# Kernel optimization log

Hardware: AMD Instinct MI355X
Metric: run time of the kernel (lower is better)

## Reference

```python
import jax, jax.numpy as jnp
import numpy as np

DEPTH = 64
N_HEAD = 8
FF = 128
EPS = 1e-5


def layer_norm(x, g, b):
    mu = jnp.mean(x, axis=-1, keepdims=True)
    var = jnp.mean((x - mu) ** 2, axis=-1, keepdims=True)
    return (x - mu) * jax.lax.rsqrt(var + EPS) * g + b


def setup_inputs() -> dict:
    key = jax.random.key(0)
    ks = jax.random.split(key, 16)
    B, S, d, h = 4, 512, DEPTH, N_HEAD
    s = 1.0 / np.sqrt(d)
    return {
        "seq": jax.random.normal(ks[0], (B, S, d), jnp.float32),
        "pos_enc": jax.random.normal(ks[1], (B, S, S, d), jnp.float32),
        "Wq": jax.random.normal(ks[2], (d, d * h), jnp.float32) * s,
        "Wk": jax.random.normal(ks[3], (d, d * h), jnp.float32) * s,
        "Wv": jax.random.normal(ks[4], (d, d * h), jnp.float32) * s,
        "Wo": jax.random.normal(ks[5], (d * h, d), jnp.float32) / np.sqrt(d * h),
        "Wp": jax.random.normal(ks[6], (d, h), jnp.float32) * s,
        "bp": jnp.zeros((h,), jnp.float32),
        "W1": jax.random.normal(ks[7], (d, FF), jnp.float32) * s,
        "b1": jnp.zeros((FF,), jnp.float32),
        "W2": jax.random.normal(ks[8], (FF, d), jnp.float32) / np.sqrt(FF),
        "b2": jnp.zeros((d,), jnp.float32),
        "g_att": jnp.ones((d,), jnp.float32),
        "b_att": jnp.zeros((d,), jnp.float32),
        "g_ff": jnp.ones((d,), jnp.float32),
        "b_ff": jnp.zeros((d,), jnp.float32),
    }


def reference(seq, pos_enc, Wq, Wk, Wv, Wo, Wp, bp, W1, b1, W2, b2, g_att, b_att, g_ff, b_ff):
    B, S, d = seq.shape
    h = N_HEAD
    # QKV: [B,S,h,d] -> [B,h,S,d]; head_dim == depth in this module
    q = (seq @ Wq).reshape(B, S, h, d).transpose(0, 2, 1, 3)
    k = (seq @ Wk).reshape(B, S, h, d).transpose(0, 2, 1, 3)
    v = (seq @ Wv).reshape(B, S, h, d).transpose(0, 2, 1, 3)
    a = jnp.einsum('bhid,bhjd->bhij', q, k) / jnp.sqrt(jnp.asarray(d, seq.dtype))
    # additive learned positional bias: [B,S,S,d] @ [d,h] -> [B,S,S,h] -> [B,h,S,S]
    p = jnp.einsum('bijd,dh->bhij', pos_enc, Wp) + bp[None, :, None, None]
    a = jax.nn.softmax(a + p, axis=-1)
    heads = jnp.einsum('bhij,bhjd->bhid', a, v)  # [B,h,S,d]
    o = heads.transpose(0, 2, 1, 3).reshape(B, S, h * d) @ Wo
    x = layer_norm(seq + o, g_att, b_att)
    y = jax.nn.relu(x @ W1 + b1) @ W2 + b2
    return layer_norm(x + y, g_ff, b_ff)
```

## Files before the change

### kernel.cpp

```cpp
#include <hip/hip_runtime.h>
#include <hip/hip_bf16.h>

#define DEPTH 64
#define NH 8
#define SEQL 512
#define BATCH 4
#define FFDIM 128
#define PROJ (DEPTH*NH)
#define LOG2E 1.44269504088896340736f

typedef __hip_bfloat16 bf16;
typedef __attribute__((ext_vector_type(8))) short short8;
typedef __attribute__((ext_vector_type(4))) float floatx4;

__device__ __forceinline__ short f2bs(float f) {
    __hip_bfloat16 h = __float2bfloat16(f);
    return *reinterpret_cast<short*>(&h);
}
__device__ __forceinline__ float bs2f(short s) {
    __hip_bfloat16 h = *reinterpret_cast<__hip_bfloat16*>(&s);
    return __bfloat162float(h);
}

__global__ __launch_bounds__(256) void qkv_kernel(
    const float* __restrict__ seq, const float* __restrict__ Wq,
    const float* __restrict__ Wk, const float* __restrict__ Wv,
    bf16* __restrict__ q, bf16* __restrict__ k, bf16* __restrict__ vT)
{
    __shared__ __align__(16) short sS[64][72];
    __shared__ __align__(16) short sW[128][72];
    __shared__ __align__(16) short sT[128][72];
    int t = threadIdx.x;
    int lane = t & 63, w = t >> 6;
    const float* W; int vflag = 0;
    bf16* out;
    if (blockIdx.z == 0)      { W = Wq; out = q; }
    else if (blockIdx.z == 1) { W = Wk; out = k; }
    else                      { W = Wv; out = vT; vflag = 1; }
    int m0 = blockIdx.x * 64;
    int n0 = blockIdx.y * 128;

    for (int idx = t; idx < 4096; idx += 256) {
        int r = idx >> 6, kk = idx & 63;
        sS[r][kk] = f2bs(seq[(long)(m0 + r)*64 + kk]);
    }
    for (int idx = t; idx < 8192; idx += 256) {
        int kk = idx >> 7, n = idx & 127;
        sW[n][kk] = f2bs(W[kk*512 + n0 + n]);
    }
    __syncthreads();

    int ln = lane & 15, g4 = lane >> 4;
    int mt = w;
    floatx4 acc[2][4];
    #pragma unroll
    for (int nh = 0; nh < 2; nh++)
        #pragma unroll
        for (int nt = 0; nt < 4; nt++) acc[nh][nt] = (floatx4){0.f,0.f,0.f,0.f};
    #pragma unroll
    for (int ks = 0; ks < 2; ks++) {
        short8 af = *(const short8*)&sS[mt*16 + ln][ks*32 + g4*8];
        #pragma unroll
        for (int nh = 0; nh < 2; nh++)
            #pragma unroll
            for (int nt = 0; nt < 4; nt++) {
                short8 bfv = *(const short8*)&sW[nh*64 + nt*16 + ln][ks*32 + g4*8];
                acc[nh][nt] = __builtin_amdgcn_mfma_f32_16x16x32_bf16(af, bfv, acc[nh][nt], 0, 0, 0);
            }
    }

    if (!vflag) {
        #pragma unroll
        for (int nh = 0; nh < 2; nh++)
            #pragma unroll
            for (int nt = 0; nt < 4; nt++)
                #pragma unroll
                for (int r = 0; r < 4; r++) {
                    int grow = m0 + mt*16 + g4*4 + r;
                    int col  = n0 + nh*64 + nt*16 + ln;
                    int b = grow >> 9, s = grow & 511;
                    int h = col >> 6, d = col & 63;
                    out[(((long)(b*8 + h)*512) + s)*64 + d] = __float2bfloat16(acc[nh][nt][r]);
                }
    } else {
        #pragma unroll
        for (int nh = 0; nh < 2; nh++)
            #pragma unroll
            for (int nt = 0; nt < 4; nt++)
                #pragma unroll
                for (int r = 0; r < 4; r++)
                    sT[nh*64 + nt*16 + ln][mt*16 + g4*4 + r] = f2bs(acc[nh][nt][r]);
        __syncthreads();
        int b = m0 >> 9, s0 = m0 & 511;
        for (int idx = t; idx < 1024; idx += 256) {
            int lc = idx >> 3, c8 = idx & 7;
            *(uint4*)(out + ((long)(b*512 + n0 + lc))*512 + s0 + c8*8) =
                *(const uint4*)&sT[lc][c8*8];
        }
    }
}

__global__ __launch_bounds__(256) void pbias_kernel(
    const float* __restrict__ pos, const float* __restrict__ Wp,
    const float* __restrict__ bp, bf16* __restrict__ p)
{
    __shared__ __align__(16) float sW2[4][132];
    __shared__ float sb[8];
    int t = threadIdx.x;
    for (int i = t; i < 512; i += 256) {
        int sub = i >> 7, rest = i & 127;
        int lk = rest >> 3, h = rest & 7;
        int kk = ((lk >> 2) << 4) + sub*4 + (lk & 3);
        sW2[sub][lk*8 + h] = Wp[kk*8 + h];
    }
    if (t < 8) sb[t] = bp[t];
    __syncthreads();

    int sub = t & 3;
    int lrow = t >> 2;
    long row = (long)blockIdx.x*64 + lrow;

    const float4* src = (const float4*)(pos + row*64);
    float4 ch[4];
    #pragma unroll
    for (int i = 0; i < 4; i++) ch[i] = src[i*4 + sub];

    float acc[8];
    #pragma unroll
    for (int h = 0; h < 8; h++) acc[h] = 0.f;
    #pragma unroll
    for (int i = 0; i < 4; i++) {
        #pragma unroll
        for (int e = 0; e < 4; e++) {
            float x = ((const float*)&ch[i])[e];
            int lk = i*4 + e;
            const float4* wr = (const float4*)&sW2[sub][lk*8];
            float4 wa = wr[0], wb = wr[1];
            acc[0] += x*wa.x; acc[1] += x*wa.y; acc[2] += x*wa.z; acc[3] += x*wa.w;
            acc[4] += x*wb.x; acc[5] += x*wb.y; acc[6] += x*wb.z; acc[7] += x*wb.w;
        }
    }
    #pragma unroll
    for (int h = 0; h < 8; h++) {
        acc[h] += __shfl_xor(acc[h], 1, 64);
        acc[h] += __shfl_xor(acc[h], 2, 64);
    }
    int b = (int)(row >> 18);
    int rem = (int)(row & 262143);
    int i = rem >> 9, j = rem & 511;
    int h1 = sub, h2 = sub + 4;
    p[(((long)(b*8 + h1)*512 + i) << 9) + j] = __float2bfloat16(acc[h1] + sb[h1]);
    p[(((long)(b*8 + h2)*512 + i) << 9) + j] = __float2bfloat16(acc[h2] + sb[h2]);
}

__global__ __launch_bounds__(256) void attn_kernel(
    const bf16* __restrict__ q, const bf16* __restrict__ k,
    const bf16* __restrict__ vT, const bf16* __restrict__ p,
    bf16* __restrict__ heads)
{
    __shared__ __align__(16) short sQ[64*72];
    __shared__ __align__(16) short sK[64*72];
    __shared__ __align__(16) short sV[64*72];
    __shared__ __align__(16) short sP[4][16*72];

    int t = threadIdx.x;
    int lane = t & 63, w = t >> 6;
    int bid = blockIdx.x;
    int it = bid & 7;
    int bh = bid >> 3;
    int i0 = it*64;

    const bf16* qb = q + ((long)bh*SEQL + i0)*DEPTH;
    const bf16* kb = k + (long)bh*SEQL*DEPTH;
    const bf16* vb = vT + (long)bh*DEPTH*SEQL;
    const bf16* pb = p + ((long)bh*SEQL + i0)*SEQL;

    for (int c = t; c < 512; c += 256) {
        int r = c >> 3, c8 = c & 7;
        *(uint4*)((char*)sQ + r*144 + c8*16) = *(const uint4*)(qb + r*64 + c8*8);
    }

    int ln = lane & 15, g4 = lane >> 4;
    float lsum[4];
    floatx4 oacc[4];
    #pragma unroll
    for (int r = 0; r < 4; r++) lsum[r] = 0.f;
    #pragma unroll
    for (int ds = 0; ds < 4; ds++) oacc[ds] = (floatx4){0.f,0.f,0.f,0.f};

    for (int jt = 0; jt < 8; jt++) {
        __syncthreads();
        int j0 = jt*64;
        for (int c = t; c < 512; c += 256) {
            int r = c >> 3, c8 = c & 7;
            *(uint4*)((char*)sK + r*144 + c8*16) = *(const uint4*)(kb + (long)(j0 + r)*64 + c8*8);
        }
        for (int c = t; c < 512; c += 256) {
            int r = c >> 3, c8 = c & 7;
            *(uint4*)((char*)sV + r*144 + c8*16) = *(const uint4*)(vb + (long)r*512 + j0 + c8*8);
        }
        __syncthreads();

        floatx4 sacc[4];
        #pragma unroll
        for (int js = 0; js < 4; js++) sacc[js] = (floatx4){0.f,0.f,0.f,0.f};
        #pragma unroll
        for (int kk = 0; kk < 2; kk++) {
            short8 aq = *(const short8*)((const char*)sQ + (w*16 + ln)*144 + kk*64 + g4*16);
            #pragma unroll
            for (int js = 0; js < 4; js++) {
                short8 bk = *(const short8*)((const char*)sK + (js*16 + ln)*144 + kk*64 + g4*16);
                sacc[js] = __builtin_amdgcn_mfma_f32_16x16x32_bf16(aq, bk, sacc[js], 0, 0, 0);
            }
        }
        #pragma unroll
        for (int js = 0; js < 4; js++)
            #pragma unroll
            for (int r = 0; r < 4; r++) {
                int gi = w*16 + g4*4 + r;
                int gj = j0 + js*16 + ln;
                float pv = __bfloat162float(pb[(long)gi*SEQL + gj]);
                float e = exp2f((sacc[js][r]*0.125f + pv)*LOG2E);
                lsum[r] += e;
                sP[w][(g4*4 + r)*72 + js*16 + ln] = f2bs(e);
            }
        #pragma unroll
        for (int kk = 0; kk < 2; kk++) {
            short8 ap = *(const short8*)((const char*)sP[w] + ln*144 + kk*64 + g4*16);
            #pragma unroll
            for (int ds = 0; ds < 4; ds++) {
                short8 bv = *(const short8*)((const char*)sV + (ds*16 + ln)*144 + kk*64 + g4*16);
                oacc[ds] = __builtin_amdgcn_mfma_f32_16x16x32_bf16(ap, bv, oacc[ds], 0, 0, 0);
            }
        }
    }

    #pragma unroll
    for (int r = 0; r < 4; r++)
        #pragma unroll
        for (int m = 1; m < 16; m <<= 1) lsum[r] += __shfl_xor(lsum[r], m, 64);

    int b = bh >> 3, h = bh & 7;
    #pragma unroll
    for (int ds = 0; ds < 4; ds++)
        #pragma unroll
        for (int r = 0; r < 4; r++) {
            float val = oacc[ds][r] / lsum[r];
            int gi = i0 + w*16 + g4*4 + r;
            int col = h*64 + ds*16 + ln;
            heads[((long)b*SEQL + gi)*PROJ + col] = __float2bfloat16(val);
        }
}

__global__ __launch_bounds__(256) void tail_kernel(
    const bf16* __restrict__ heads, const float* __restrict__ Wo,
    const float* __restrict__ seq, const float* __restrict__ g_att,
    const float* __restrict__ b_att, const float* __restrict__ W1,
    const float* __restrict__ b1, const float* __restrict__ W2,
    const float* __restrict__ b2, const float* __restrict__ g_ff,
    const float* __restrict__ b_ff, float* __restrict__ out)
{
    __shared__ __align__(16) short sH[4][520];
    __shared__ float sX[4][68];
    __shared__ float sHid[4][132];
    int t = threadIdx.x;
    int w = t >> 6, lane = t & 63;
    long g0 = (long)blockIdx.x*4;
    {
        int r = t >> 6, c8 = t & 63;
        *(uint4*)((char*)&sH[r][0] + c8*16) = *(const uint4*)(heads + (g0 + r)*PROJ + c8*8);
    }
    float acc = 0.f;
    #pragma unroll 8
    for (int kk = 0; kk < PROJ; kk++) {
        float hv = bs2f(sH[w][kk]);
        acc += hv * Wo[kk*DEPTH + lane];
    }
    long row = g0 + w;
    float x0 = acc + seq[row*DEPTH + lane];
    float s1 = x0, s2 = x0*x0;
    #pragma unroll
    for (int m = 1; m < 64; m <<= 1) { s1 += __shfl_xor(s1, m, 64); s2 += __shfl_xor(s2, m, 64); }
    float mu = s1*(1.f/64.f);
    float var = s2*(1.f/64.f) - mu*mu;
    float rstd = rsqrtf(var + 1e-5f);
    float xn = (x0 - mu)*rstd*g_att[lane] + b_att[lane];
    sX[w][lane] = xn;

    float h0 = b1[lane], h1 = b1[lane + 64];
    #pragma unroll 8
    for (int kk = 0; kk < DEPTH; kk++) {
        float xv = sX[w][kk];
        h0 += xv * W1[kk*FFDIM + lane];
        h1 += xv * W1[kk*FFDIM + 64 + lane];
    }
    h0 = fmaxf(h0, 0.f); h1 = fmaxf(h1, 0.f);
    sHid[w][lane] = h0; sHid[w][lane + 64] = h1;

    float acc2 = b2[lane];
    #pragma unroll 8
    for (int kk = 0; kk < FFDIM; kk++)
        acc2 += sHid[w][kk] * W2[kk*DEPTH + lane];

    float z = xn + acc2;
    float t1 = z, t2 = z*z;
    #pragma unroll
    for (int m = 1; m < 64; m <<= 1) { t1 += __shfl_xor(t1, m, 64); t2 += __shfl_xor(t2, m, 64); }
    float mu2 = t1*(1.f/64.f);
    float var2 = t2*(1.f/64.f) - mu2*mu2;
    float rstd2 = rsqrtf(var2 + 1e-5f);
    out[row*DEPTH + lane] = (z - mu2)*rstd2*g_ff[lane] + b_ff[lane];
}

extern "C" void kernel_launch(void* const* d_in, const int* in_sizes, int n_in,
                              void* d_out, int out_size, void* d_ws, size_t ws_size,
                              hipStream_t stream) {
    const float* seq   = (const float*)d_in[0];
    const float* pos   = (const float*)d_in[1];
    const float* Wq    = (const float*)d_in[2];
    const float* Wk    = (const float*)d_in[3];
    const float* Wv    = (const float*)d_in[4];
    const float* Wo    = (const float*)d_in[5];
    const float* Wp    = (const float*)d_in[6];
    const float* bp    = (const float*)d_in[7];
    const float* W1    = (const float*)d_in[8];
    const float* b1    = (const float*)d_in[9];
    const float* W2    = (const float*)d_in[10];
    const float* b2    = (const float*)d_in[11];
    const float* g_att = (const float*)d_in[12];
    const float* b_att = (const float*)d_in[13];
    const float* g_ff  = (const float*)d_in[14];
    const float* b_ff  = (const float*)d_in[15];
    float* outp = (float*)d_out;

    bf16* qb  = (bf16*)d_ws;
    bf16* kb  = qb + 1048576;
    bf16* vTb = kb + 1048576;
    bf16* pb  = vTb + 1048576;
    bf16* hb  = pb + 8388608;

    qkv_kernel  <<<dim3(32, 4, 3), 256, 0, stream>>>(seq, Wq, Wk, Wv, qb, kb, vTb);
    pbias_kernel<<<16384,          256, 0, stream>>>(pos, Wp, bp, pb);
    attn_kernel <<<256,            256, 0, stream>>>(qb, kb, vTb, pb, hb);
    tail_kernel <<<512,            256, 0, stream>>>(hb, Wo, seq, g_att, b_att,
                                                     W1, b1, W2, b2, g_ff, b_ff, outp);
}
```

Before: 112.9 us.

## Merge QKV and pos-bias kernels, shrink attention tiles, prefetch bias, batch tail rows

Merges the QKV projection and the positional-bias projection into one launch, with block ranges dispatched by block index and shared memory overlapped through a union. This removes one kernel launch and lets both parts run concurrently. The attention kernel switches to 32-row query tiles with 128 threads, giving twice as many blocks, and prefetches the next tile's bias values into registers during the K/V loop. The tail kernel has each wave process two rows so every Wo/W1/W2 weight load is reused twice. Together these add register pressure and change occupancy.

```diff
diff --git a/kernel.cpp b/kernel.cpp
--- a/kernel.cpp
+++ b/kernel.cpp
@@ -22,160 +22,164 @@
     return __bfloat162float(h);
 }
 
-__global__ __launch_bounds__(256) void qkv_kernel(
+__global__ __launch_bounds__(256) void front_kernel(
     const float* __restrict__ seq, const float* __restrict__ Wq,
     const float* __restrict__ Wk, const float* __restrict__ Wv,
-    bf16* __restrict__ q, bf16* __restrict__ k, bf16* __restrict__ vT)
+    const float* __restrict__ pos, const float* __restrict__ Wp,
+    const float* __restrict__ bp,
+    bf16* __restrict__ q, bf16* __restrict__ k, bf16* __restrict__ vT,
+    bf16* __restrict__ p)
 {
-    __shared__ __align__(16) short sS[64][72];
-    __shared__ __align__(16) short sW[128][72];
-    __shared__ __align__(16) short sT[128][72];
+    __shared__ __align__(16) union {
+        struct { short sS[64][72]; short sW[128][72]; } g;
+        struct { float sW2[4][132]; float sb[8]; } pb;
+    } U;
     int t = threadIdx.x;
-    int lane = t & 63, w = t >> 6;
-    const float* W; int vflag = 0;
-    bf16* out;
-    if (blockIdx.z == 0)      { W = Wq; out = q; }
-    else if (blockIdx.z == 1) { W = Wk; out = k; }
-    else                      { W = Wv; out = vT; vflag = 1; }
-    int m0 = blockIdx.x * 64;
-    int n0 = blockIdx.y * 128;
-
-    for (int idx = t; idx < 4096; idx += 256) {
-        int r = idx >> 6, kk = idx & 63;
-        sS[r][kk] = f2bs(seq[(long)(m0 + r)*64 + kk]);
-    }
-    for (int idx = t; idx < 8192; idx += 256) {
-        int kk = idx >> 7, n = idx & 127;
-        sW[n][kk] = f2bs(W[kk*512 + n0 + n]);
-    }
-    __syncthreads();
-
-    int ln = lane & 15, g4 = lane >> 4;
-    int mt = w;
-    floatx4 acc[2][4];
-    #pragma unroll
-    for (int nh = 0; nh < 2; nh++)
-        #pragma unroll
-        for (int nt = 0; nt < 4; nt++) acc[nh][nt] = (floatx4){0.f,0.f,0.f,0.f};
-    #pragma unroll
-    for (int ks = 0; ks < 2; ks++) {
-        short8 af = *(const short8*)&sS[mt*16 + ln][ks*32 + g4*8];
+    int bid = blockIdx.x;
+
+    if (bid < 384) {
+        int lane = t & 63, w = t >> 6;
+        int z = bid >> 7, rem = bid & 127;
+        int mi = rem & 31, ni = rem >> 5;
+        const float* W; int vflag = 0; bf16* out;
+        if (z == 0)      { W = Wq; out = q; }
+        else if (z == 1) { W = Wk; out = k; }
+        else             { W = Wv; out = vT; vflag = 1; }
+        int m0 = mi * 64;
+        int n0 = ni * 128;
+
+        for (int idx = t; idx < 4096; idx += 256) {
+            int r = idx >> 6, kk = idx & 63;
+            U.g.sS[r][kk] = f2bs(seq[(long)(m0 + r)*64 + kk]);
+        }
+        for (int idx = t; idx < 8192; idx += 256) {
+            int kk = idx >> 7, n = idx & 127;
+            U.g.sW[n][kk] = f2bs(W[kk*512 + n0 + n]);
+        }
+        __syncthreads();
+
+        int ln = lane & 15, g4 = lane >> 4;
+        int mt = w;
+        floatx4 acc[2][4];
         #pragma unroll
         for (int nh = 0; nh < 2; nh++)
             #pragma unroll
-            for (int nt = 0; nt < 4; nt++) {
-                short8 bfv = *(const short8*)&sW[nh*64 + nt*16 + ln][ks*32 + g4*8];
-                acc[nh][nt] = __builtin_amdgcn_mfma_f32_16x16x32_bf16(af, bfv, acc[nh][nt], 0, 0, 0);
-            }
-    }
-
-    if (!vflag) {
-        #pragma unroll
-        for (int nh = 0; nh < 2; nh++)
-            #pragma unroll
-            for (int nt = 0; nt < 4; nt++)
+            for (int nt = 0; nt < 4; nt++) acc[nh][nt] = (floatx4){0.f,0.f,0.f,0.f};
+        #pragma unroll
+        for (int ks = 0; ks < 2; ks++) {
+            short8 af = *(const short8*)&U.g.sS[mt*16 + ln][ks*32 + g4*8];
+            #pragma unroll
+            for (int nh = 0; nh < 2; nh++)
                 #pragma unroll
-                for (int r = 0; r < 4; r++) {
-                    int grow = m0 + mt*16 + g4*4 + r;
-                    int col  = n0 + nh*64 + nt*16 + ln;
-                    int b = grow >> 9, s = grow & 511;
-                    int h = col >> 6, d = col & 63;
-                    out[(((long)(b*8 + h)*512) + s)*64 + d] = __float2bfloat16(acc[nh][nt][r]);
+                for (int nt = 0; nt < 4; nt++) {
+                    short8 bfv = *(const short8*)&U.g.sW[nh*64 + nt*16 + ln][ks*32 + g4*8];
+                    acc[nh][nt] = __builtin_amdgcn_mfma_f32_16x16x32_bf16(af, bfv, acc[nh][nt], 0, 0, 0);
                 }
+        }
+
+        if (!vflag) {
+            #pragma unroll
+            for (int nh = 0; nh < 2; nh++)
+                #pragma unroll
+                for (int nt = 0; nt < 4; nt++)
+                    #pragma unroll
+                    for (int r = 0; r < 4; r++) {
+                        int grow = m0 + mt*16 + g4*4 + r;
+                        int col  = n0 + nh*64 + nt*16 + ln;
+                        int b = grow >> 9, s = grow & 511;
+                        int h = col >> 6, d = col & 63;
+                        out[(((long)(b*8 + h)*512) + s)*64 + d] = __float2bfloat16(acc[nh][nt][r]);
+                    }
+        } else {
+            __syncthreads();
+            short (*sT)[72] = U.g.sW;
+            #pragma unroll
+            for (int nh = 0; nh < 2; nh++)
+                #pragma unroll
+                for (int nt = 0; nt < 4; nt++)
+                    #pragma unroll
+                    for (int r = 0; r < 4; r++)
+                        sT[nh*64 + nt*16 + ln][mt*16 + g4*4 + r] = f2bs(acc[nh][nt][r]);
+            __syncthreads();
+            int b = m0 >> 9, s0 = m0 & 511;
+            for (int idx = t; idx < 1024; idx += 256) {
+                int lc = idx >> 3, c8 = idx & 7;
+                *(uint4*)(out + ((long)(b*512 + n0 + lc))*512 + s0 + c8*8) =
+                    *(const uint4*)&sT[lc][c8*8];
+            }
+        }
     } else {
-        #pragma unroll
-        for (int nh = 0; nh < 2; nh++)
-            #pragma unroll
-            for (int nt = 0; nt < 4; nt++)
-                #pragma unroll
-                for (int r = 0; r < 4; r++)
-                    sT[nh*64 + nt*16 + ln][mt*16 + g4*4 + r] = f2bs(acc[nh][nt][r]);
+        int pid = bid - 384;
+        for (int i = t; i < 512; i += 256) {
+            int sub = i >> 7, rest = i & 127;
+            int lk = rest >> 3, h = rest & 7;
+            int kk = ((lk >> 2) << 4) + sub*4 + (lk & 3);
+            U.pb.sW2[sub][lk*8 + h] = Wp[kk*8 + h];
+        }
+        if (t < 8) U.pb.sb[t] = bp[t];
         __syncthreads();
-        int b = m0 >> 9, s0 = m0 & 511;
-        for (int idx = t; idx < 1024; idx += 256) {
-            int lc = idx >> 3, c8 = idx & 7;
-            *(uint4*)(out + ((long)(b*512 + n0 + lc))*512 + s0 + c8*8) =
-                *(const uint4*)&sT[lc][c8*8];
-        }
-    }
-}
-
-__global__ __launch_bounds__(256) void pbias_kernel(
-    const float* __restrict__ pos, const float* __restrict__ Wp,
-    const float* __restrict__ bp, bf16* __restrict__ p)
-{
-    __shared__ __align__(16) float sW2[4][132];
-    __shared__ float sb[8];
-    int t = threadIdx.x;
-    for (int i = t; i < 512; i += 256) {
-        int sub = i >> 7, rest = i & 127;
-        int lk = rest >> 3, h = rest & 7;
-        int kk = ((lk >> 2) << 4) + sub*4 + (lk & 3);
-        sW2[sub][lk*8 + h] = Wp[kk*8 + h];
-    }
-    if (t < 8) sb[t] = bp[t];
-    __syncthreads();
-
-    int sub = t & 3;
-    int lrow = t >> 2;
-    long row = (long)blockIdx.x*64 + lrow;
-
-    const float4* src = (const float4*)(pos + row*64);
-    float4 ch[4];
-    #pragma unroll
-    for (int i = 0; i < 4; i++) ch[i] = src[i*4 + sub];
-
-    float acc[8];
-    #pragma unroll
-    for (int h = 0; h < 8; h++) acc[h] = 0.f;
-    #pragma unroll
-    for (int i = 0; i < 4; i++) {
-        #pragma unroll
-        for (int e = 0; e < 4; e++) {
-            float x = ((const float*)&ch[i])[e];
-            int lk = i*4 + e;
-            const float4* wr = (const float4*)&sW2[sub][lk*8];
-            float4 wa = wr[0], wb = wr[1];
-            acc[0] += x*wa.x; acc[1] += x*wa.y; acc[2] += x*wa.z; acc[3] += x*wa.w;
-            acc[4] += x*wb.x; acc[5] += x*wb.y; acc[6] += x*wb.z; acc[7] += x*wb.w;
-        }
-    }
-    #pragma unroll
-    for (int h = 0; h < 8; h++) {
-        acc[h] += __shfl_xor(acc[h], 1, 64);
-        acc[h] += __shfl_xor(acc[h], 2, 64);
-    }
-    int b = (int)(row >> 18);
-    int rem = (int)(row & 262143);
-    int i = rem >> 9, j = rem & 511;
-    int h1 = sub, h2 = sub + 4;
-    p[(((long)(b*8 + h1)*512 + i) << 9) + j] = __float2bfloat16(acc[h1] + sb[h1]);
-    p[(((long)(b*8 + h2)*512 + i) << 9) + j] = __float2bfloat16(acc[h2] + sb[h2]);
-}
-
-__global__ __launch_bounds__(256) void attn_kernel(
+
+        int sub = t & 3;
+        int lrow = t >> 2;
+        long row = (long)pid*64 + lrow;
+
+        const float4* src = (const float4*)(pos + row*64);
+        float4 ch[4];
+        #pragma unroll
+        for (int i = 0; i < 4; i++) ch[i] = src[i*4 + sub];
+
+        float acc[8];
+        #pragma unroll
+        for (int h = 0; h < 8; h++) acc[h] = 0.f;
+        #pragma unroll
+        for (int i = 0; i < 4; i++) {
+            #pragma unroll
+            for (int e = 0; e < 4; e++) {
+                float x = ((const float*)&ch[i])[e];
+                int lk = i*4 + e;
+                const float4* wr = (const float4*)&U.pb.sW2[sub][lk*8];
+                float4 wa = wr[0], wb = wr[1];
+                acc[0] += x*wa.x; acc[1] += x*wa.y; acc[2] += x*wa.z; acc[3] += x*wa.w;
+                acc[4] += x*wb.x; acc[5] += x*wb.y; acc[6] += x*wb.z; acc[7] += x*wb.w;
+            }
+        }
+        #pragma unroll
+        for (int h = 0; h < 8; h++) {
+            acc[h] += __shfl_xor(acc[h], 1, 64);
+            acc[h] += __shfl_xor(acc[h], 2, 64);
+        }
+        int b = (int)(row >> 18);
+        int rem = (int)(row & 262143);
+        int i = rem >> 9, j = rem & 511;
+        int h1 = sub, h2 = sub + 4;
+        p[(((long)(b*8 + h1)*512 + i) << 9) + j] = __float2bfloat16(acc[h1] + U.pb.sb[h1]);
+        p[(((long)(b*8 + h2)*512 + i) << 9) + j] = __float2bfloat16(acc[h2] + U.pb.sb[h2]);
+    }
+}
+
+__global__ __launch_bounds__(128) void attn_kernel(
     const bf16* __restrict__ q, const bf16* __restrict__ k,
     const bf16* __restrict__ vT, const bf16* __restrict__ p,
     bf16* __restrict__ heads)
 {
-    __shared__ __align__(16) short sQ[64*72];
+    __shared__ __align__(16) short sQ[32*72];
     __shared__ __align__(16) short sK[64*72];
     __shared__ __align__(16) short sV[64*72];
-    __shared__ __align__(16) short sP[4][16*72];
+    __shared__ __align__(16) short sP[2][16*72];
 
     int t = threadIdx.x;
     int lane = t & 63, w = t >> 6;
     int bid = blockIdx.x;
-    int it = bid & 7;
-    int bh = bid >> 3;
-    int i0 = it*64;
+    int it = bid & 15;
+    int bh = bid >> 4;
+    int i0 = it*32;
 
     const bf16* qb = q + ((long)bh*SEQL + i0)*DEPTH;
     const bf16* kb = k + (long)bh*SEQL*DEPTH;
     const bf16* vb = vT + (long)bh*DEPTH*SEQL;
     const bf16* pb = p + ((long)bh*SEQL + i0)*SEQL;
 
-    for (int c = t; c < 512; c += 256) {
+    for (int c = t; c < 256; c += 128) {
         int r = c >> 3, c8 = c & 7;
         *(uint4*)((char*)sQ + r*144 + c8*16) = *(const uint4*)(qb + r*64 + c8*8);
     }
@@ -188,18 +192,38 @@
     #pragma unroll
     for (int ds = 0; ds < 4; ds++) oacc[ds] = (floatx4){0.f,0.f,0.f,0.f};
 
+    unsigned short pf[16];
+    #pragma unroll
+    for (int js = 0; js < 4; js++)
+        #pragma unroll
+        for (int r = 0; r < 4; r++)
+            pf[js*4 + r] = *(const unsigned short*)&pb[(long)(w*16 + g4*4 + r)*SEQL + js*16 + ln];
+
+    #pragma unroll
     for (int jt = 0; jt < 8; jt++) {
         __syncthreads();
         int j0 = jt*64;
-        for (int c = t; c < 512; c += 256) {
+        for (int c = t; c < 512; c += 128) {
             int r = c >> 3, c8 = c & 7;
             *(uint4*)((char*)sK + r*144 + c8*16) = *(const uint4*)(kb + (long)(j0 + r)*64 + c8*8);
         }
-        for (int c = t; c < 512; c += 256) {
+        for (int c = t; c < 512; c += 128) {
             int r = c >> 3, c8 = c & 7;
             *(uint4*)((char*)sV + r*144 + c8*16) = *(const uint4*)(vb + (long)r*512 + j0 + c8*8);
         }
         __syncthreads();
+
+        unsigned short cur[16];
+        #pragma unroll
+        for (int e = 0; e < 16; e++) cur[e] = pf[e];
+        if (jt < 7) {
+            int jn = (jt + 1)*64;
+            #pragma unroll
+            for (int js = 0; js < 4; js++)
+                #pragma unroll
+                for (int r = 0; r < 4; r++)
+                    pf[js*4 + r] = *(const unsigned short*)&pb[(long)(w*16 + g4*4 + r)*SEQL + jn + js*16 + ln];
+        }
 
         floatx4 sacc[4];
         #pragma unroll
@@ -217,9 +241,7 @@
         for (int js = 0; js < 4; js++)
             #pragma unroll
             for (int r = 0; r < 4; r++) {
-                int gi = w*16 + g4*4 + r;
-                int gj = j0 + js*16 + ln;
-                float pv = __bfloat162float(pb[(long)gi*SEQL + gj]);
+                float pv = bs2f((short)cur[js*4 + r]);
                 float e = exp2f((sacc[js][r]*0.125f + pv)*LOG2E);
                 lsum[r] += e;
                 sP[w][(g4*4 + r)*72 + js*16 + ln] = f2bs(e);
@@ -260,56 +282,82 @@
     const float* __restrict__ b2, const float* __restrict__ g_ff,
     const float* __restrict__ b_ff, float* __restrict__ out)
 {
-    __shared__ __align__(16) short sH[4][520];
-    __shared__ float sX[4][68];
-    __shared__ float sHid[4][132];
+    __shared__ __align__(16) short sH[8][520];
+    __shared__ float sX[8][68];
+    __shared__ float sHid[8][132];
     int t = threadIdx.x;
     int w = t >> 6, lane = t & 63;
-    long g0 = (long)blockIdx.x*4;
-    {
-        int r = t >> 6, c8 = t & 63;
+    long g0 = (long)blockIdx.x*8;
+
+    for (int idx = t; idx < 512; idx += 256) {
+        int r = idx >> 6, c8 = idx & 63;
         *(uint4*)((char*)&sH[r][0] + c8*16) = *(const uint4*)(heads + (g0 + r)*PROJ + c8*8);
     }
-    float acc = 0.f;
-    #pragma unroll 8
-    for (int kk = 0; kk < PROJ; kk++) {
-        float hv = bs2f(sH[w][kk]);
-        acc += hv * Wo[kk*DEPTH + lane];
-    }
-    long row = g0 + w;
-    float x0 = acc + seq[row*DEPTH + lane];
-    float s1 = x0, s2 = x0*x0;
-    #pragma unroll
-    for (int m = 1; m < 64; m <<= 1) { s1 += __shfl_xor(s1, m, 64); s2 += __shfl_xor(s2, m, 64); }
-    float mu = s1*(1.f/64.f);
-    float var = s2*(1.f/64.f) - mu*mu;
-    float rstd = rsqrtf(var + 1e-5f);
-    float xn = (x0 - mu)*rstd*g_att[lane] + b_att[lane];
-    sX[w][lane] = xn;
-
-    float h0 = b1[lane], h1 = b1[lane + 64];
-    #pragma unroll 8
+    __syncthreads();
+
+    int r0 = w*2, r1 = w*2 + 1;
+    float acc0 = 0.f, acc1 = 0.f;
+    #pragma unroll 4
+    for (int kk8 = 0; kk8 < 64; kk8++) {
+        short8 a0 = *(const short8*)&sH[r0][kk8*8];
+        short8 a1 = *(const short8*)&sH[r1][kk8*8];
+        #pragma unroll
+        for (int e = 0; e < 8; e++) {
+            float wv = Wo[(kk8*8 + e)*DEPTH + lane];
+            acc0 += bs2f(a0[e])*wv;
+            acc1 += bs2f(a1[e])*wv;
+        }
+    }
+    float ga = g_att[lane], ba = b_att[lane];
+    float xn[2];
+    #pragma unroll
+    for (int rr = 0; rr < 2; rr++) {
+        long row = g0 + w*2 + rr;
+        float x0 = (rr ? acc1 : acc0) + seq[row*DEPTH + lane];
+        float s1 = x0, s2 = x0*x0;
+        #pragma unroll
+        for (int m = 1; m < 64; m <<= 1) { s1 += __shfl_xor(s1, m, 64); s2 += __shfl_xor(s2, m, 64); }
+        float mu = s1*(1.f/64.f);
+        float var = s2*(1.f/64.f) - mu*mu;
+        float rstd = rsqrtf(var + 1e-5f);
+        xn[rr] = (x0 - mu)*rstd*ga + ba;
+        sX[w*2 + rr][lane] = xn[rr];
+    }
+
+    float b1a = b1[lane], b1b = b1[lane + 64];
+    float h00 = b1a, h01 = b1b, h10 = b1a, h11 = b1b;
+    #pragma unroll 4
     for (int kk = 0; kk < DEPTH; kk++) {
-        float xv = sX[w][kk];
-        h0 += xv * W1[kk*FFDIM + lane];
-        h1 += xv * W1[kk*FFDIM + 64 + lane];
-    }
-    h0 = fmaxf(h0, 0.f); h1 = fmaxf(h1, 0.f);
-    sHid[w][lane] = h0; sHid[w][lane + 64] = h1;
-
-    float acc2 = b2[lane];
-    #pragma unroll 8
-    for (int kk = 0; kk < FFDIM; kk++)
-        acc2 += sHid[w][kk] * W2[kk*DEPTH + lane];
-
-    float z = xn + acc2;
-    float t1 = z, t2 = z*z;
-    #pragma unroll
-    for (int m = 1; m < 64; m <<= 1) { t1 += __shfl_xor(t1, m, 64); t2 += __shfl_xor(t2, m, 64); }
-    float mu2 = t1*(1.f/64.f);
-    float var2 = t2*(1.f/64.f) - mu2*mu2;
-    float rstd2 = rsqrtf(var2 + 1e-5f);
-    out[row*DEPTH + lane] = (z - mu2)*rstd2*g_ff[lane] + b_ff[lane];
+        float w0 = W1[kk*FFDIM + lane];
+        float w1 = W1[kk*FFDIM + 64 + lane];
+        float x0v = sX[r0][kk], x1v = sX[r1][kk];
+        h00 += x0v*w0; h01 += x0v*w1;
+        h10 += x1v*w0; h11 += x1v*w1;
+    }
+    sHid[r0][lane] = fmaxf(h00, 0.f); sHid[r0][lane + 64] = fmaxf(h01, 0.f);
+    sHid[r1][lane] = fmaxf(h10, 0.f); sHid[r1][lane + 64] = fmaxf(h11, 0.f);
+
+    float bb = b2[lane];
+    float acc20 = bb, acc21 = bb;
+    #pragma unroll 4
+    for (int kk = 0; kk < FFDIM; kk++) {
+        float wv = W2[kk*DEPTH + lane];
+        acc20 += sHid[r0][kk]*wv;
+        acc21 += sHid[r1][kk]*wv;
+    }
+    float gf = g_ff[lane], bf = b_ff[lane];
+    #pragma unroll
+    for (int rr = 0; rr < 2; rr++) {
+        long row = g0 + w*2 + rr;
+        float z = xn[rr] + (rr ? acc21 : acc20);
+        float t1 = z, t2 = z*z;
+        #pragma unroll
+        for (int m = 1; m < 64; m <<= 1) { t1 += __shfl_xor(t1, m, 64); t2 += __shfl_xor(t2, m, 64); }
+        float mu2 = t1*(1.f/64.f);
+        float var2 = t2*(1.f/64.f) - mu2*mu2;
+        float rstd2 = rsqrtf(var2 + 1e-5f);
+        out[row*DEPTH + lane] = (z - mu2)*rstd2*gf + bf;
+    }
 }
 
 extern "C" void kernel_launch(void* const* d_in, const int* in_sizes, int n_in,
@@ -339,9 +387,9 @@
     bf16* pb  = vTb + 1048576;
     bf16* hb  = pb + 8388608;
 
-    qkv_kernel  <<<dim3(32, 4, 3), 256, 0, stream>>>(seq, Wq, Wk, Wv, qb, kb, vTb);
-    pbias_kernel<<<16384,          256, 0, stream>>>(pos, Wp, bp, pb);
-    attn_kernel <<<256,            256, 0, stream>>>(qb, kb, vTb, pb, hb);
-    tail_kernel <<<512,            256, 0, stream>>>(hb, Wo, seq, g_att, b_att,
-                                                     W1, b1, W2, b2, g_ff, b_ff, outp);
-}
+    front_kernel<<<16768, 256, 0, stream>>>(seq, Wq, Wk, Wv, pos, Wp, bp,
+                                            qb, kb, vTb, pb);
+    attn_kernel <<<512,   128, 0, stream>>>(qb, kb, vTb, pb, hb);
+    tail_kernel <<<256,   256, 0, stream>>>(hb, Wo, seq, g_att, b_att,
+                                            W1, b1, W2, b2, g_ff, b_ff, outp);
+}
```

Measured after the change: 121.3 us. +7.5%, slower.
